# Optimization experiments

Hardware: AMD Instinct MI355X
Metric: run time of the kernel (lower is better)

## Reference

```python
import jax, jax.numpy as jnp
from jax import lax
import numpy as np

N, M, P, K = 2, 16384, 5023, 4
C_PLANE, HP = 32, 256
OUT_DIM = 32


def _harmonic(x):
    # pytorch3d HarmonicEmbedding(n=4, logspace, omega_0=1, append_input=True)
    f = jnp.asarray([1.0, 2.0, 4.0, 8.0], x.dtype)
    e = (x[..., None] * f).reshape(x.shape[:-1] + (-1,))  # [..., 12]
    return jnp.concatenate([jnp.sin(e), jnp.cos(e), x], axis=-1)  # [..., 27]


def _grid_sample2d(img, grid):
    # img [C,H,W], grid [M,2] (x->W, y->H) in [-1,1]; bilinear, zero pad, align_corners=False
    C, H, W = img.shape
    x = (grid[:, 0] + 1.0) * (W / 2.0) - 0.5
    y = (grid[:, 1] + 1.0) * (H / 2.0) - 0.5
    x0 = jnp.floor(x); y0 = jnp.floor(y)
    x1 = x0 + 1.0; y1 = y0 + 1.0
    wx1 = x - x0; wx0 = 1.0 - wx1
    wy1 = y - y0; wy0 = 1.0 - wy1
    def gather(ix, iy):
        valid = ((ix >= 0) & (ix < W) & (iy >= 0) & (iy < H)).astype(img.dtype)
        ixc = jnp.clip(ix, 0, W - 1).astype(jnp.int32)
        iyc = jnp.clip(iy, 0, H - 1).astype(jnp.int32)
        return img[:, iyc, ixc] * valid[None, :]  # [C,M]
    out = (gather(x0, y0) * (wx0 * wy0) + gather(x1, y0) * (wx1 * wy0)
           + gather(x0, y1) * (wx0 * wy1) + gather(x1, y1) * (wx1 * wy1))
    return out.T  # [M,C]


def _forward(coordinates, directions, points_position, tex_tplanes, emb_table,
             pw1, pb1, pw2, pb2, fw1, fb1, fw2, fb2, fw3, fb3, dw, db, rw1, rb1, rw2, rb2):
    c = coordinates
    p = points_position
    # --- triplane sampling (EG3D projections (x,y),(x,z),(z,x)), mean over planes ---
    proj = jnp.stack([c[..., :2],
                      c[..., jnp.array([0, 2])],
                      c[..., jnp.array([2, 0])]], axis=1)  # [N,3,M,2]
    tex = jax.vmap(jax.vmap(_grid_sample2d))(tex_tplanes, proj).mean(axis=1)  # [N,M,32]
    # --- KNN (squared distances, ascending, as pytorch3d knn_points) ---
    d2 = (jnp.sum(c * c, -1)[:, :, None] + jnp.sum(p * p, -1)[:, None, :]
          - 2.0 * jnp.einsum('nmc,npc->nmp', c, p))  # [N,M,P]
    negd, idx = lax.top_k(-d2, K)
    dist = -negd  # [N,M,K]
    nn = jax.vmap(lambda pts, i: pts[i])(p, idx)  # [N,M,K,3]
    pf = emb_table[idx]  # [N,M,K,32]
    rel = c[:, :, None, :] - nn
    rel = rel / jnp.maximum(jnp.linalg.norm(rel, axis=-1, keepdims=True), 1e-12)
    h = jnp.concatenate([pf, _harmonic(rel)], axis=-1)  # [N,M,K,59]
    h = jax.nn.relu(h @ pw1 + pb1) @ pw2 + pb2  # [N,M,K,32]
    w = 1.0 / dist
    w = w / jnp.sum(w, axis=1, keepdims=True)  # dim=1 exactly as in source
    pts_feat = jnp.sum(h * w[..., None], axis=2)  # [N,M,32]
    # --- dense MLP stack ---
    feat = jnp.concatenate([tex, pts_feat], axis=-1)  # [N,M,64]
    feat = jax.nn.relu(feat @ fw1 + fb1)
    feat = jax.nn.relu(feat @ fw2 + fb2)
    feat = feat @ fw3 + fb3  # [N,M,128]
    selector = jnp.all((c > -1.0) & (c < 1.0), axis=-1)  # [N,M]
    raw = (jax.nn.softplus(10.0 * (feat @ dw + db)) / 10.0) * selector[..., None]
    densities = 1.0 - jnp.exp(-raw)
    rays = directions / jnp.maximum(jnp.linalg.norm(directions, axis=-1, keepdims=True), 1e-12)
    rgb = jnp.concatenate([feat, _harmonic(rays)], axis=-1)  # [N,M,155]
    rgb = jax.nn.relu(rgb @ rw1 + rb1) @ rw2 + rb2  # [N,M,OUT_DIM]
    rgb = jnp.concatenate([jax.nn.sigmoid(rgb[..., :3]) * (1.0 + 2 * 0.001) - 0.001,
                           rgb[..., 3:]], axis=-1)
    return densities, rgb, dist


def setup_inputs() -> dict:
    key = jax.random.key(0)
    ks = jax.random.split(key, 16)
    rn = lambda k, s, sc=1.0: jax.random.normal(k, s, jnp.float32) * sc
    def lin(k, i, o):
        k1, k2 = jax.random.split(k)
        return rn(k1, (i, o), 1.0 / np.sqrt(i)), rn(k2, (o,), 0.01)
    coordinates = jax.random.uniform(ks[0], (N, M, 3), jnp.float32)
    directions = rn(ks[1], (N, M, 3))
    points_position = jax.random.uniform(ks[2], (N, P, 3), jnp.float32)
    tex_tplanes = rn(ks[3], (N, 3, C_PLANE, HP, HP))
    emb_table = rn(ks[4], (P, 32), 0.02)
    pw1, pb1 = lin(ks[5], 32 + 27, 64)
    pw2, pb2 = lin(ks[6], 64, 32)
    fw1, fb1 = lin(ks[7], 64, 128)
    fw2, fb2 = lin(ks[8], 128, 128)
    fw3, fb3 = lin(ks[9], 128, 128)
    dw, db = lin(ks[10], 128, 1)
    rw1, rb1 = lin(ks[11], 128 + 27, 64)
    rw2, rb2 = lin(ks[12], 64, OUT_DIM)
    return dict(coordinates=coordinates, directions=directions, points_position=points_position,
                tex_tplanes=tex_tplanes, emb_table=emb_table, pw1=pw1, pb1=pb1, pw2=pw2, pb2=pb2,
                fw1=fw1, fb1=fb1, fw2=fw2, fb2=fb2, fw3=fw3, fb3=fb3, dw=dw, db=db,
                rw1=rw1, rb1=rb1, rw2=rw2, rb2=rb2)


def reference(coordinates, directions, points_position, tex_tplanes, emb_table,
              pw1, pb1, pw2, pb2, fw1, fb1, fw2, fb2, fw3, fb3, dw, db, rw1, rb1, rw2, rb2):
    return _forward(coordinates, directions, points_position, tex_tplanes, emb_table,
                    pw1, pb1, pw2, pb2, fw1, fb1, fw2, fb2, fw3, fb3, dw, db, rw1, rb1, rw2, rb2)
```

## Files before the change

### kernel.cpp

```cpp
#include <hip/hip_runtime.h>
#include <float.h>
#include <math.h>

#define NB 2
#define MQ 16384
#define NQ (NB*MQ)
#define PP 5023
#define KNN 4
#define HPX 256
#define HWSZ (HPX*HPX)

#define OUT_RGB_OFF  ((size_t)NQ)
#define OUT_DIST_OFF ((size_t)NQ + (size_t)NQ*32)

#define WS_SUMS_OFF ((size_t)NQ*KNN*4)
#define WS_PTS4_OFF ((size_t)0x90000)
#define WS_WP_OFF   ((size_t)0xC0000)
#define WS_TEX_OFF  ((size_t)1<<20)

#define WP_PW1 0
#define WP_PW2 1920
#define WP_FW1 2944
#define WP_FW2 7040
#define WP_FW3 15232
#define WP_DW  23424
#define WP_RW1 23488
#define WP_RW2 28480

typedef __attribute__((ext_vector_type(2))) _Float16 half2v;

static __device__ __forceinline__ unsigned int pk2(float a, float b) {
    half2v h; h[0] = (_Float16)a; h[1] = (_Float16)b;
    return __builtin_bit_cast(unsigned int, h);
}
static __device__ __forceinline__ float2 upk(unsigned int u) {
    half2v h = __builtin_bit_cast(half2v, u);
    return make_float2((float)h[0], (float)h[1]);
}
static __device__ __forceinline__ float dot2(unsigned int a, unsigned int b, float c) {
    return __builtin_amdgcn_fdot2(__builtin_bit_cast(half2v, a),
                                  __builtin_bit_cast(half2v, b), c, false);
}

struct PackArgs {
    const float* src[8];
    int off[8]; int din[8]; int dout[8];
};
__global__ __launch_bounds__(256) void k_pack(PackArgs a, unsigned int* wp) {
    const int mid = blockIdx.y;
    const int idx = blockIdx.x * 256 + threadIdx.x;
    const int DIN = a.din[mid], DOUT = a.dout[mid];
    const int din2 = (DIN + 1) >> 1;
    if (idx >= din2 * DOUT) return;
    const int i2 = idx / DOUT, j = idx - i2 * DOUT;
    const float* s = a.src[mid];
    const float lo = s[(2*i2) * DOUT + j];
    const float hi = (2*i2 + 1 < DIN) ? s[(2*i2 + 1) * DOUT + j] : 0.f;
    wp[a.off[mid] + idx] = pk2(lo, hi);
}

__global__ __launch_bounds__(256) void k_pts4(const float* __restrict__ pts,
                                              float4* __restrict__ o) {
    const int i = blockIdx.x * 256 + threadIdx.x;
    if (i >= NB * PP) return;
    const float px = pts[3*i], py = pts[3*i+1], pz = pts[3*i+2];
    o[i] = make_float4(px, py, pz, fmaf(px, px, fmaf(py, py, pz*pz)));
}

__global__ __launch_bounds__(256) void k_transpose(const float* __restrict__ src,
                                                   float* __restrict__ dst) {
    const int tid = threadIdx.x;
    const int b = blockIdx.x;
    const int n3 = b >> 8;
    const int hw = ((b & 255) << 8) + tid;
    const float* s = src + (size_t)n3 * 32 * HWSZ + hw;
    float v[32];
#pragma unroll
    for (int c = 0; c < 32; ++c) v[c] = s[(size_t)c * HWSZ];
    float4* d = (float4*)(dst + ((size_t)n3 * HWSZ + hw) * 32);
#pragma unroll
    for (int c = 0; c < 8; ++c) d[c] = make_float4(v[4*c], v[4*c+1], v[4*c+2], v[4*c+3]);
}

__global__ __launch_bounds__(1024, 2) void k_knn(const float* __restrict__ coords,
                                                 const float4* __restrict__ pts4,
                                                 const float* __restrict__ pts,
                                                 float* __restrict__ odist,
                                                 int* __restrict__ oidx) {
    __shared__ unsigned int KB[16][4][64];
    const int tid  = threadIdx.x;
    const int lane = tid & 63;
    const int w    = __builtin_amdgcn_readfirstlane(tid >> 6);
    const int q0   = blockIdx.x * 64;
    const int q    = q0 + lane;
    const int n    = q0 >> 14;
    const float cx = coords[q*3+0], cy = coords[q*3+1], cz = coords[q*3+2];
    const float cc = fmaf(cx, cx, fmaf(cy, cy, cz*cz));
    const float4* __restrict__ p4 = pts4 + (size_t)n * PP;

    const int chunk  = (PP + 15) / 16;
    const int pstart = w * chunk;
    const int pend   = (pstart + chunk < PP) ? (pstart + chunk) : PP;

    unsigned int k0 = 0xFFFFFFFFu, k1 = 0xFFFFFFFFu, k2 = 0xFFFFFFFFu, k3 = 0xFFFFFFFFu;

#define INS(kb) { \
        unsigned int m2 = ((kb) > k2) ? (kb) : k2;  k3 = (k3 < m2) ? k3 : m2; \
        unsigned int m1 = ((kb) > k1) ? (kb) : k1;  k2 = (k2 < m1) ? k2 : m1; \
        unsigned int m0 = ((kb) > k0) ? (kb) : k0;  k1 = (k1 < m0) ? k1 : m0; \
        k0 = (k0 < (kb)) ? k0 : (kb); }

    int p = pstart;
    for (; p + 8 <= pend; p += 8) {
        float4 P[8];
#pragma unroll
        for (int j = 0; j < 8; ++j) P[j] = p4[p + j];
#pragma unroll
        for (int j = 0; j < 8; ++j) {
            const float dot = fmaf(cx, P[j].x, fmaf(cy, P[j].y, cz * P[j].z));
            float dd = fmaxf(fmaf(-2.0f, dot, cc + P[j].w), 0.f);
            const unsigned int kb = (__float_as_uint(dd) & 0xFFFFE000u) | (unsigned int)(p + j);
            INS(kb)
        }
    }
    for (; p < pend; ++p) {
        const float4 P = p4[p];
        const float dot = fmaf(cx, P.x, fmaf(cy, P.y, cz * P.z));
        float dd = fmaxf(fmaf(-2.0f, dot, cc + P.w), 0.f);
        const unsigned int kb = (__float_as_uint(dd) & 0xFFFFE000u) | (unsigned int)p;
        INS(kb)
    }

    KB[w][0][lane] = k0; KB[w][1][lane] = k1; KB[w][2][lane] = k2; KB[w][3][lane] = k3;
    __syncthreads();

    if (w == 0) {
        unsigned int s0 = 0xFFFFFFFFu, s1 = 0xFFFFFFFFu, s2 = 0xFFFFFFFFu, s3 = 0xFFFFFFFFu;
#pragma unroll
        for (int ww = 0; ww < 16; ++ww)
#pragma unroll
            for (int j = 0; j < 4; ++j) {
                const unsigned int kb = KB[ww][j][lane];
                unsigned int m2 = (kb > s2) ? kb : s2;  s3 = (s3 < m2) ? s3 : m2;
                unsigned int m1 = (kb > s1) ? kb : s1;  s2 = (s2 < m1) ? s2 : m1;
                unsigned int m0 = (kb > s0) ? kb : s0;  s1 = (s1 < m0) ? s1 : m0;
                s0 = (s0 < kb) ? s0 : kb;
            }
        const float* __restrict__ pb = pts + (size_t)n * PP * 3;
        int   id[4] = { (int)(s0 & 0x1FFFu), (int)(s1 & 0x1FFFu),
                        (int)(s2 & 0x1FFFu), (int)(s3 & 0x1FFFu) };
        float dv[4];
#pragma unroll
        for (int j = 0; j < 4; ++j) {
            const float px = pb[3*id[j]+0], py = pb[3*id[j]+1], pz = pb[3*id[j]+2];
            const float dt  = fmaf(cx, px, fmaf(cy, py, cz*pz));
            const float pp2 = fmaf(px, px, fmaf(py, py, pz*pz));
            dv[j] = fmaf(-2.0f, dt, cc + pp2);
        }
#define CSW(a,b) { bool sw = (dv[b] < dv[a]) || (dv[b] == dv[a] && id[b] < id[a]); \
                   if (sw) { float td=dv[a]; dv[a]=dv[b]; dv[b]=td; int ti=id[a]; id[a]=id[b]; id[b]=ti; } }
        CSW(0,1) CSW(2,3) CSW(0,2) CSW(1,3) CSW(1,2)
#undef CSW
        *(float4*)(odist + (size_t)q*4) = make_float4(dv[0], dv[1], dv[2], dv[3]);
        *(int4*)(oidx + (size_t)q*4)    = make_int4(id[0], id[1], id[2], id[3]);
    }
#undef INS
}

__global__ __launch_bounds__(1024) void k_sums(const float* __restrict__ dist,
                                               float* __restrict__ sums) {
    const int b = blockIdx.x;
    const int n = b >> 2, k = b & 3;
    float s = 0.f;
    for (int m = threadIdx.x; m < MQ; m += 1024)
        s += 1.0f / dist[((size_t)n * MQ + m) * 4 + k];
    __shared__ float red[1024];
    red[threadIdx.x] = s;
    __syncthreads();
    for (int off = 512; off > 0; off >>= 1) {
        if (threadIdx.x < off) red[threadIdx.x] += red[threadIdx.x + off];
        __syncthreads();
    }
    if (threadIdx.x == 0) sums[b] = red[0];
}

template<int DIN2, int DOUT, int TILE>
__device__ __forceinline__ void gemv_p(const unsigned int* __restrict__ Xp, int lane,
                                       const unsigned int* __restrict__ Wp,
                                       const float* __restrict__ bias,
                                       int j0, float (&acc)[TILE]) {
#pragma unroll
    for (int u = 0; u < TILE; ++u) acc[u] = bias[j0 + u];
#pragma unroll
    for (int i2 = 0; i2 < DIN2; ++i2) {
        const unsigned int xv = Xp[i2 * 64 + lane];
        const unsigned int* wr = Wp + i2 * DOUT + j0;
#pragma unroll
        for (int u = 0; u < TILE; ++u) acc[u] = dot2(xv, wr[u], acc[u]);
    }
}

static __device__ __forceinline__ float harm_val(int h, float rx, float ry, float rz) {
    if (h >= 27) return 0.f;
    float v;
    if (h < 24) {
        int base = (h < 12) ? h : (h - 12);
        float rv = (base >> 2) == 0 ? rx : ((base >> 2) == 1 ? ry : rz);
        float e = rv * (float)(1 << (base & 3));
        v = (h < 12) ? sinf(e) : cosf(e);
    } else {
        v = (h == 24) ? rx : ((h == 25) ? ry : rz);
    }
    return v;
}

__global__ __launch_bounds__(1024, 2) void k_main(
    const float* __restrict__ coords, const float* __restrict__ dirs,
    const float* __restrict__ pts, const float* __restrict__ tex_raw,
    const float* __restrict__ tex_t, const float* __restrict__ emb,
    const unsigned int* __restrict__ wp,
    const float* __restrict__ pb1, const float* __restrict__ pb2,
    const float* __restrict__ fb1, const float* __restrict__ fb2,
    const float* __restrict__ fb3, const float* __restrict__ db,
    const float* __restrict__ rb1, const float* __restrict__ rb2,
    const int* __restrict__ idxbuf, const float* __restrict__ distbuf,
    const float* __restrict__ sums, float* __restrict__ out, int use_tex_t)
{
    __shared__ unsigned int S[248 * 64];
    const int tid  = threadIdx.x;
    const int lane = tid & 63;
    const int wv   = __builtin_amdgcn_readfirstlane(tid >> 6);
    const int q0   = blockIdx.x * 64;
    const int n    = q0 >> 14;
    const int q    = q0 + lane;

    float tex_acc[2] = {0.f, 0.f};
    {
        const int g = wv;
        const float cx = coords[q*3+0], cy = coords[q*3+1], cz = coords[q*3+2];
#pragma unroll
        for (int pl = 0; pl < 3; ++pl) {
            float gx = (pl == 2) ? cz : cx;
            float gy = (pl == 0) ? cy : ((pl == 1) ? cz : cx);
            float x = (gx + 1.f) * 128.f - 0.5f;
            float y = (gy + 1.f) * 128.f - 0.5f;
            float x0f = floorf(x), y0f = floorf(y);
            float wx1 = x - x0f, wy1 = y - y0f;
            float wx0 = 1.f - wx1, wy0 = 1.f - wy1;
            int x0 = (int)x0f, y0 = (int)y0f;
            int n3 = n * 3 + pl;
            int  xs[4] = { x0, x0+1, x0,   x0+1 };
            int  ys[4] = { y0, y0,   y0+1, y0+1 };
            float wt[4] = { wx0*wy0, wx1*wy0, wx0*wy1, wx1*wy1 };
#pragma unroll
            for (int c = 0; c < 4; ++c) {
                int xi = xs[c], yi = ys[c];
                if (xi >= 0 && xi < HPX && yi >= 0 && yi < HPX) {
                    float wgt = wt[c];
                    if (use_tex_t) {
                        const float2 a = *(const float2*)(tex_t +
                            (((size_t)n3 * HWSZ + (size_t)yi * HPX + xi) * 32 + g * 2));
                        tex_acc[0] = fmaf(wgt, a.x, tex_acc[0]);
                        tex_acc[1] = fmaf(wgt, a.y, tex_acc[1]);
                    } else {
                        size_t base = ((size_t)(n3 * 32 + g * 2)) * HWSZ + (size_t)yi * HPX + xi;
                        tex_acc[0] = fmaf(wgt, tex_raw[base], tex_acc[0]);
                        tex_acc[1] = fmaf(wgt, tex_raw[base + HWSZ], tex_acc[1]);
                    }
                }
            }
        }
        tex_acc[0] *= (1.f / 3.f); tex_acc[1] *= (1.f / 3.f);
    }

    const int kk  = wv & 3;
    const int prt = wv >> 2;

    {
        const int id = idxbuf[(size_t)q*4 + kk];
        const int rb = kk * 30;
        if (prt < 2) {
#pragma unroll
            for (int t = 0; t < 2; ++t) {
                const float4 e = *(const float4*)(emb + (size_t)id * 32 + prt*16 + t*4 + 0)
                    , e2 = *(const float4*)(emb + (size_t)id * 32 + prt*16 + t*4 + 8);
                S[(rb + prt*8 + t*2    )*64 + lane] = pk2(e.x,  e.y);
                S[(rb + prt*8 + t*2 + 1)*64 + lane] = pk2(e.z,  e.w);
                S[(rb + prt*8 + t*2 + 4)*64 + lane] = pk2(e2.x, e2.y);
                S[(rb + prt*8 + t*2 + 5)*64 + lane] = pk2(e2.z, e2.w);
            }
        } else {
            const float cx = coords[q*3+0], cy = coords[q*3+1], cz = coords[q*3+2];
            const float nx = pts[((size_t)n*PP + id)*3 + 0];
            const float ny = pts[((size_t)n*PP + id)*3 + 1];
            const float nz = pts[((size_t)n*PP + id)*3 + 2];
            float rx = cx - nx, ry = cy - ny, rz = cz - nz;
            float nrm = sqrtf(fmaf(rx, rx, fmaf(ry, ry, rz*rz)));
            float inv = 1.f / fmaxf(nrm, 1e-12f);
            rx *= inv; ry *= inv; rz *= inv;
            const int pr0 = (prt == 2) ? 0 : 8;
            const int prn = (prt == 2) ? 8 : 6;
#pragma unroll
            for (int t = 0; t < 8; ++t) {
                if (t < prn) {
                    int pr = pr0 + t;
                    S[(rb + 16 + pr)*64 + lane] =
                        pk2(harm_val(2*pr, rx, ry, rz), harm_val(2*pr + 1, rx, ry, rz));
                }
            }
        }
    }
    __syncthreads();

    {
        float acc[16];
        gemv_p<30, 64, 16>(S + (kk*30)*64, lane, wp + WP_PW1, pb1, prt * 16, acc);
        const int rb = 120 + kk*32 + prt*8;
#pragma unroll
        for (int u = 0; u < 8; ++u)
            S[(rb + u)*64 + lane] = pk2(fmaxf(acc[2*u], 0.f), fmaxf(acc[2*u+1], 0.f));
    }
    __syncthreads();

    {
        float acc[8];
        gemv_p<32, 32, 8>(S + (120 + kk*32)*64, lane, wp + WP_PW2, pb2, prt * 8, acc);
        const float dist = distbuf[(size_t)q*4 + kk];
        const float wk = (1.0f / dist) / sums[n*4 + kk];
        const int rb = kk*16 + prt*4;
#pragma unroll
        for (int u = 0; u < 4; ++u)
            S[(rb + u)*64 + lane] = pk2(wk * acc[2*u], wk * acc[2*u+1]);
    }
    __syncthreads();

    {
        S[(128 + wv)*64 + lane] = pk2(tex_acc[0], tex_acc[1]);
        float a = 0.f, b = 0.f;
#pragma unroll
        for (int k = 0; k < 4; ++k) {
            float2 v = upk(S[(k*16 + wv)*64 + lane]);
            a += v.x; b += v.y;
        }
        S[(144 + wv)*64 + lane] = pk2(a, b);
    }
    __syncthreads();

    {
        float acc[8];
        gemv_p<32, 128, 8>(S + 128*64, lane, wp + WP_FW1, fb1, wv * 8, acc);
#pragma unroll
        for (int u = 0; u < 4; ++u)
            S[(4*wv + u)*64 + lane] = pk2(fmaxf(acc[2*u], 0.f), fmaxf(acc[2*u+1], 0.f));
    }
    __syncthreads();
    {
        float acc[8];
        gemv_p<64, 128, 8>(S, lane, wp + WP_FW2, fb2, wv * 8, acc);
#pragma unroll
        for (int u = 0; u < 4; ++u)
            S[(64 + 4*wv + u)*64 + lane] = pk2(fmaxf(acc[2*u], 0.f), fmaxf(acc[2*u+1], 0.f));
    }
    __syncthreads();
    {
        float acc[8];
        gemv_p<64, 128, 8>(S + 64*64, lane, wp + WP_FW3, fb3, wv * 8, acc);
#pragma unroll
        for (int u = 0; u < 4; ++u)
            S[(4*wv + u)*64 + lane] = pk2(acc[2*u], acc[2*u+1]);
    }
    __syncthreads();
    {
        if (wv < 14) {
            float dx = dirs[q*3+0], dy = dirs[q*3+1], dz = dirs[q*3+2];
            float dn = sqrtf(fmaf(dx, dx, fmaf(dy, dy, dz*dz)));
            float inv = 1.f / fmaxf(dn, 1e-12f);
            dx *= inv; dy *= inv; dz *= inv;
            S[(128 + wv)*64 + lane] = pk2(harm_val(2*wv, dx, dy, dz),
                                          harm_val(2*wv + 1, dx, dy, dz));
        } else if (wv == 15) {
            float z = db[0];
            const unsigned int* dwp = wp + WP_DW;
#pragma unroll
            for (int i2 = 0; i2 < 64; ++i2) z = dot2(S[i2*64 + lane], dwp[i2], z);
            const float cx = coords[q*3+0], cy = coords[q*3+1], cz = coords[q*3+2];
            float selv = (cx > -1.f && cx < 1.f && cy > -1.f && cy < 1.f &&
                          cz > -1.f && cz < 1.f) ? 1.f : 0.f;
            float t10 = 10.f * z;
            float sp = (t10 > 20.f) ? t10 : log1pf(expf(t10));
            float raw = sp * 0.1f * selv;
            out[q] = 1.f - expf(-raw);
        }
    }
    __syncthreads();
    {
        const int j0 = wv * 4;
        float acc[4];
        gemv_p<64, 64, 4>(S, lane, wp + WP_RW1, rb1, j0, acc);
#pragma unroll
        for (int t = 0; t < 14; ++t) {
            const unsigned int xv = S[(128 + t)*64 + lane];
            const unsigned int* wr = wp + WP_RW1 + (64 + t) * 64 + j0;
#pragma unroll
            for (int u = 0; u < 4; ++u) acc[u] = dot2(xv, wr[u], acc[u]);
        }
        S[(64 + 2*wv    )*64 + lane] = pk2(fmaxf(acc[0], 0.f), fmaxf(acc[1], 0.f));
        S[(64 + 2*wv + 1)*64 + lane] = pk2(fmaxf(acc[2], 0.f), fmaxf(acc[3], 0.f));
    }
    __syncthreads();
    {
        float acc[2];
        gemv_p<32, 32, 2>(S + 64*64, lane, wp + WP_RW2, rb2, wv * 2, acc);
#pragma unroll
        for (int u = 0; u < 2; ++u) {
            int j = wv*2 + u;
            float v = acc[u];
            if (j < 3) v = 1.002f * (1.f / (1.f + expf(-v))) - 0.001f;
            out[OUT_RGB_OFF + (size_t)q*32 + j] = v;
        }
    }
}

extern "C" void kernel_launch(void* const* d_in, const int* in_sizes, int n_in,
                              void* d_out, int out_size, void* d_ws, size_t ws_size,
                              hipStream_t stream) {
    (void)in_sizes; (void)n_in; (void)out_size;
    const float* coords = (const float*)d_in[0];
    const float* dirs   = (const float*)d_in[1];
    const float* pts    = (const float*)d_in[2];
    const float* tex    = (const float*)d_in[3];
    const float* emb    = (const float*)d_in[4];
    const float* pw1 = (const float*)d_in[5];  const float* pb1 = (const float*)d_in[6];
    const float* pw2 = (const float*)d_in[7];  const float* pb2 = (const float*)d_in[8];
    const float* fw1 = (const float*)d_in[9];  const float* fb1 = (const float*)d_in[10];
    const float* fw2 = (const float*)d_in[11]; const float* fb2 = (const float*)d_in[12];
    const float* fw3 = (const float*)d_in[13]; const float* fb3 = (const float*)d_in[14];
    const float* dw  = (const float*)d_in[15]; const float* db  = (const float*)d_in[16];
    const float* rw1 = (const float*)d_in[17]; const float* rb1 = (const float*)d_in[18];
    const float* rw2 = (const float*)d_in[19]; const float* rb2 = (const float*)d_in[20];

    float*        out    = (float*)d_out;
    int*          wsidx  = (int*)d_ws;
    float*        wssums = (float*)((char*)d_ws + WS_SUMS_OFF);
    float4*       wspts4 = (float4*)((char*)d_ws + WS_PTS4_OFF);
    unsigned int* wswp   = (unsigned int*)((char*)d_ws + WS_WP_OFF);
    float*        wstex  = (float*)((char*)d_ws + WS_TEX_OFF);

    const size_t need_tex = WS_TEX_OFF + (size_t)6 * HWSZ * 32 * 4;
    const int use_t = (ws_size >= need_tex) ? 1 : 0;

    PackArgs pa;
    pa.src[0] = pw1; pa.off[0] = WP_PW1; pa.din[0] = 59;  pa.dout[0] = 64;
    pa.src[1] = pw2; pa.off[1] = WP_PW2; pa.din[1] = 64;  pa.dout[1] = 32;
    pa.src[2] = fw1; pa.off[2] = WP_FW1; pa.din[2] = 64;  pa.dout[2] = 128;
    pa.src[3] = fw2; pa.off[3] = WP_FW2; pa.din[3] = 128; pa.dout[3] = 128;
    pa.src[4] = fw3; pa.off[4] = WP_FW3; pa.din[4] = 128; pa.dout[4] = 128;
    pa.src[5] = dw;  pa.off[5] = WP_DW;  pa.din[5] = 128; pa.dout[5] = 1;
    pa.src[6] = rw1; pa.off[6] = WP_RW1; pa.din[6] = 155; pa.dout[6] = 64;
    pa.src[7] = rw2; pa.off[7] = WP_RW2; pa.din[7] = 64;  pa.dout[7] = 32;

    k_pack<<<dim3(32, 8), 256, 0, stream>>>(pa, wswp);
    k_pts4<<<(NB*PP + 255)/256, 256, 0, stream>>>(pts, wspts4);
    if (use_t) k_transpose<<<6 * 256, 256, 0, stream>>>(tex, wstex);
    k_knn<<<NQ / 64, 1024, 0, stream>>>(coords, wspts4, pts, out + OUT_DIST_OFF, wsidx);
    k_sums<<<8, 1024, 0, stream>>>(out + OUT_DIST_OFF, wssums);
    k_main<<<NQ / 64, 1024, 0, stream>>>(coords, dirs, pts, tex, wstex, emb,
                                         wswp, pb1, pb2, fb1, fb2, fb3, db, rb1, rb2,
                                         wsidx, out + OUT_DIST_OFF, wssums, out, use_t);
}
```

Measured before the change: 330.4 us.

## Stage KNN points and MLP weights in LDS with double-buffered prefetch

The KNN kernel now loads point chunks cooperatively into shared memory and scans them from LDS rather than each wave streaming from global memory. The main MLP kernel copies weight slices into two shared buffers through register prefetch interleaved with compute, so GEMV weight reads come from LDS instead of scalar or global loads. It also processes the K neighbors two at a time to shrink the activation buffer. This adds many more barriers, a longer serial schedule and more LDS use, which may reduce occupancy.

```diff
diff --git a/kernel.cpp b/kernel.cpp
--- a/kernel.cpp
+++ b/kernel.cpp
@@ -82,11 +82,13 @@
     for (int c = 0; c < 8; ++c) d[c] = make_float4(v[4*c], v[4*c+1], v[4*c+2], v[4*c+3]);
 }
 
+#define KCHUNK 2560
 __global__ __launch_bounds__(1024, 2) void k_knn(const float* __restrict__ coords,
                                                  const float4* __restrict__ pts4,
                                                  const float* __restrict__ pts,
                                                  float* __restrict__ odist,
                                                  int* __restrict__ oidx) {
+    __shared__ float4 SP[KCHUNK];
     __shared__ unsigned int KB[16][4][64];
     const int tid  = threadIdx.x;
     const int lane = tid & 63;
@@ -98,10 +100,6 @@
     const float cc = fmaf(cx, cx, fmaf(cy, cy, cz*cz));
     const float4* __restrict__ p4 = pts4 + (size_t)n * PP;
 
-    const int chunk  = (PP + 15) / 16;
-    const int pstart = w * chunk;
-    const int pend   = (pstart + chunk < PP) ? (pstart + chunk) : PP;
-
     unsigned int k0 = 0xFFFFFFFFu, k1 = 0xFFFFFFFFu, k2 = 0xFFFFFFFFu, k3 = 0xFFFFFFFFu;
 
 #define INS(kb) { \
@@ -110,26 +108,27 @@
         unsigned int m0 = ((kb) > k0) ? (kb) : k0;  k1 = (k1 < m0) ? k1 : m0; \
         k0 = (k0 < (kb)) ? k0 : (kb); }
 
-    int p = pstart;
-    for (; p + 8 <= pend; p += 8) {
-        float4 P[8];
-#pragma unroll
-        for (int j = 0; j < 8; ++j) P[j] = p4[p + j];
-#pragma unroll
-        for (int j = 0; j < 8; ++j) {
-            const float dot = fmaf(cx, P[j].x, fmaf(cy, P[j].y, cz * P[j].z));
-            float dd = fmaxf(fmaf(-2.0f, dot, cc + P[j].w), 0.f);
-            const unsigned int kb = (__float_as_uint(dd) & 0xFFFFE000u) | (unsigned int)(p + j);
+#pragma unroll 1
+    for (int half = 0; half < 2; ++half) {
+        const int base = half * KCHUNK;
+        const int cnt  = (PP - base < KCHUNK) ? (PP - base) : KCHUNK;
+        __syncthreads();
+        for (int i = tid; i < cnt; i += 1024) SP[i] = p4[base + i];
+        __syncthreads();
+        const int per = (cnt + 15) >> 4;
+        const int s0 = w * per;
+        const int s1 = (s0 + per < cnt) ? (s0 + per) : cnt;
+#pragma unroll 4
+        for (int j = s0; j < s1; ++j) {
+            const float4 P = SP[j];
+            const float dot = fmaf(cx, P.x, fmaf(cy, P.y, cz * P.z));
+            float dd = fmaxf(fmaf(-2.0f, dot, cc + P.w), 0.f);
+            const unsigned int kb = (__float_as_uint(dd) & 0xFFFFE000u)
+                                    | (unsigned int)(base + j);
             INS(kb)
         }
     }
-    for (; p < pend; ++p) {
-        const float4 P = p4[p];
-        const float dot = fmaf(cx, P.x, fmaf(cy, P.y, cz * P.z));
-        float dd = fmaxf(fmaf(-2.0f, dot, cc + P.w), 0.f);
-        const unsigned int kb = (__float_as_uint(dd) & 0xFFFFE000u) | (unsigned int)p;
-        INS(kb)
-    }
+#undef INS
 
     KB[w][0][lane] = k0; KB[w][1][lane] = k1; KB[w][2][lane] = k2; KB[w][3][lane] = k3;
     __syncthreads();
@@ -164,7 +163,6 @@
         *(float4*)(odist + (size_t)q*4) = make_float4(dv[0], dv[1], dv[2], dv[3]);
         *(int4*)(oidx + (size_t)q*4)    = make_int4(id[0], id[1], id[2], id[3]);
     }
-#undef INS
 }
 
 __global__ __launch_bounds__(1024) void k_sums(const float* __restrict__ dist,
@@ -185,8 +183,8 @@
 }
 
 template<int DIN2, int DOUT, int TILE>
-__device__ __forceinline__ void gemv_p(const unsigned int* __restrict__ Xp, int lane,
-                                       const unsigned int* __restrict__ Wp,
+__device__ __forceinline__ void gemv_p(const unsigned int* Xp, int lane,
+                                       const unsigned int* Wl,
                                        const float* __restrict__ bias,
                                        int j0, float (&acc)[TILE]) {
 #pragma unroll
@@ -194,7 +192,19 @@
 #pragma unroll
     for (int i2 = 0; i2 < DIN2; ++i2) {
         const unsigned int xv = Xp[i2 * 64 + lane];
-        const unsigned int* wr = Wp + i2 * DOUT + j0;
+        const unsigned int* wr = Wl + i2 * DOUT + j0;
+#pragma unroll
+        for (int u = 0; u < TILE; ++u) acc[u] = dot2(xv, wr[u], acc[u]);
+    }
+}
+template<int DIN2, int DOUT, int TILE>
+__device__ __forceinline__ void gemv_acc(const unsigned int* Xp, int lane,
+                                         const unsigned int* Wl,
+                                         int j0, float (&acc)[TILE]) {
+#pragma unroll
+    for (int i2 = 0; i2 < DIN2; ++i2) {
+        const unsigned int xv = Xp[i2 * 64 + lane];
+        const unsigned int* wr = Wl + i2 * DOUT + j0;
 #pragma unroll
         for (int u = 0; u < TILE; ++u) acc[u] = dot2(xv, wr[u], acc[u]);
     }
@@ -226,13 +236,17 @@
     const int* __restrict__ idxbuf, const float* __restrict__ distbuf,
     const float* __restrict__ sums, float* __restrict__ out, int use_tex_t)
 {
-    __shared__ unsigned int S[248 * 64];
+    __shared__ unsigned int S[188 * 64];
+    __shared__ unsigned int WBa[2048];
+    __shared__ unsigned int WBb[2048];
     const int tid  = threadIdx.x;
     const int lane = tid & 63;
     const int wv   = __builtin_amdgcn_readfirstlane(tid >> 6);
     const int q0   = blockIdx.x * 64;
     const int n    = q0 >> 14;
     const int q    = q0 + lane;
+
+    unsigned int pa0, pa1, pb0_, pb1_;
 
     float tex_acc[2] = {0.f, 0.f};
     {
@@ -273,116 +287,210 @@
         tex_acc[0] *= (1.f / 3.f); tex_acc[1] *= (1.f / 3.f);
     }
 
-    const int kk  = wv & 3;
-    const int prt = wv >> 2;
-
+#define PF_LOAD(r0, r1, off, len) { \
+        r0 = (tid < (len)) ? wp[(off) + tid] : 0u; \
+        r1 = (tid + 1024 < (len)) ? wp[(off) + tid + 1024] : 0u; }
+#define PF_STORE(buf, r0, r1, len) { \
+        if (tid < (len)) buf[tid] = r0; \
+        if (tid + 1024 < (len)) buf[tid + 1024] = r1; }
+
+    const int kk2 = wv & 1;
+    const int sl  = wv >> 1;
+
+#define PHASE_A(pp) { \
+        const int k = (pp)*2 + kk2; \
+        const int id = idxbuf[(size_t)q*4 + k]; \
+        const int xb = 64 + kk2*30; \
+        if (sl < 4) { \
+            const float4 e0 = *(const float4*)(emb + (size_t)id * 32 + sl*8); \
+            const float4 e1 = *(const float4*)(emb + (size_t)id * 32 + sl*8 + 4); \
+            S[(xb + sl*4 + 0)*64 + lane] = pk2(e0.x, e0.y); \
+            S[(xb + sl*4 + 1)*64 + lane] = pk2(e0.z, e0.w); \
+            S[(xb + sl*4 + 2)*64 + lane] = pk2(e1.x, e1.y); \
+            S[(xb + sl*4 + 3)*64 + lane] = pk2(e1.z, e1.w); \
+        } else { \
+            const float cx = coords[q*3+0], cy = coords[q*3+1], cz = coords[q*3+2]; \
+            const float nx = pts[((size_t)n*PP + id)*3 + 0]; \
+            const float ny = pts[((size_t)n*PP + id)*3 + 1]; \
+            const float nz = pts[((size_t)n*PP + id)*3 + 2]; \
+            float rx = cx - nx, ry = cy - ny, rz = cz - nz; \
+            float nrm = sqrtf(fmaf(rx, rx, fmaf(ry, ry, rz*rz))); \
+            float inv = 1.f / fmaxf(nrm, 1e-12f); \
+            rx *= inv; ry *= inv; rz *= inv; \
+            const int pr0 = (sl == 4) ? 0 : (sl == 5) ? 4 : (sl == 6) ? 8 : 11; \
+            const int prn = (sl <= 5) ? 4 : 3; \
+            for (int t = 0; t < 4; ++t) if (t < prn) { \
+                int pr = pr0 + t; \
+                S[(xb + 16 + pr)*64 + lane] = \
+                    pk2(harm_val(2*pr, rx, ry, rz), harm_val(2*pr + 1, rx, ry, rz)); \
+            } \
+        } }
+
+#define PHASE_B() { \
+        float acc[8]; \
+        gemv_p<30, 64, 8>(S + (64 + kk2*30)*64, lane, WBa, pb1, sl*8, acc); \
+        const int rb = 124 + kk2*32 + sl*4; \
+        for (int u = 0; u < 4; ++u) \
+            S[(rb + u)*64 + lane] = pk2(fmaxf(acc[2*u], 0.f), fmaxf(acc[2*u+1], 0.f)); }
+
+#define PHASE_C(pp) { \
+        float acc[4]; \
+        gemv_p<32, 32, 4>(S + (124 + kk2*32)*64, lane, WBb, pb2, sl*4, acc); \
+        const int k = (pp)*2 + kk2; \
+        const float dist = distbuf[(size_t)q*4 + k]; \
+        const float wk = (1.0f / dist) / sums[n*4 + k]; \
+        const int rb = k*16 + sl*2; \
+        S[(rb + 0)*64 + lane] = pk2(wk * acc[0], wk * acc[1]); \
+        S[(rb + 1)*64 + lane] = pk2(wk * acc[2], wk * acc[3]); }
+
+    PF_LOAD(pa0, pa1, WP_PW1, 1920)
+    PHASE_A(0)
+    PF_STORE(WBa, pa0, pa1, 1920)
+    PF_LOAD(pb0_, pb1_, WP_PW2, 1024)
+    __syncthreads();
+    PHASE_B()
+    PF_STORE(WBb, pb0_, pb1_, 1024)
+    PF_LOAD(pa0, pa1, WP_FW1, 2048)
+    __syncthreads();
+    PHASE_C(0)
+    PHASE_A(1)
+    __syncthreads();
+    PHASE_B()
+    PF_LOAD(pb0_, pb1_, WP_FW1 + 2048, 2048)
+    __syncthreads();
+    PHASE_C(1)
+    PF_STORE(WBa, pa0, pa1, 2048)
+    __syncthreads();
     {
-        const int id = idxbuf[(size_t)q*4 + kk];
-        const int rb = kk * 30;
-        if (prt < 2) {
-#pragma unroll
-            for (int t = 0; t < 2; ++t) {
-                const float4 e = *(const float4*)(emb + (size_t)id * 32 + prt*16 + t*4 + 0)
-                    , e2 = *(const float4*)(emb + (size_t)id * 32 + prt*16 + t*4 + 8);
-                S[(rb + prt*8 + t*2    )*64 + lane] = pk2(e.x,  e.y);
-                S[(rb + prt*8 + t*2 + 1)*64 + lane] = pk2(e.z,  e.w);
-                S[(rb + prt*8 + t*2 + 4)*64 + lane] = pk2(e2.x, e2.y);
-                S[(rb + prt*8 + t*2 + 5)*64 + lane] = pk2(e2.z, e2.w);
-            }
-        } else {
-            const float cx = coords[q*3+0], cy = coords[q*3+1], cz = coords[q*3+2];
-            const float nx = pts[((size_t)n*PP + id)*3 + 0];
-            const float ny = pts[((size_t)n*PP + id)*3 + 1];
-            const float nz = pts[((size_t)n*PP + id)*3 + 2];
-            float rx = cx - nx, ry = cy - ny, rz = cz - nz;
-            float nrm = sqrtf(fmaf(rx, rx, fmaf(ry, ry, rz*rz)));
-            float inv = 1.f / fmaxf(nrm, 1e-12f);
-            rx *= inv; ry *= inv; rz *= inv;
-            const int pr0 = (prt == 2) ? 0 : 8;
-            const int prn = (prt == 2) ? 8 : 6;
-#pragma unroll
-            for (int t = 0; t < 8; ++t) {
-                if (t < prn) {
-                    int pr = pr0 + t;
-                    S[(rb + 16 + pr)*64 + lane] =
-                        pk2(harm_val(2*pr, rx, ry, rz), harm_val(2*pr + 1, rx, ry, rz));
-                }
-            }
-        }
-    }
-    __syncthreads();
-
-    {
-        float acc[16];
-        gemv_p<30, 64, 16>(S + (kk*30)*64, lane, wp + WP_PW1, pb1, prt * 16, acc);
-        const int rb = 120 + kk*32 + prt*8;
-#pragma unroll
-        for (int u = 0; u < 8; ++u)
-            S[(rb + u)*64 + lane] = pk2(fmaxf(acc[2*u], 0.f), fmaxf(acc[2*u+1], 0.f));
-    }
-    __syncthreads();
-
-    {
-        float acc[8];
-        gemv_p<32, 32, 8>(S + (120 + kk*32)*64, lane, wp + WP_PW2, pb2, prt * 8, acc);
-        const float dist = distbuf[(size_t)q*4 + kk];
-        const float wk = (1.0f / dist) / sums[n*4 + kk];
-        const int rb = kk*16 + prt*4;
-#pragma unroll
-        for (int u = 0; u < 4; ++u)
-            S[(rb + u)*64 + lane] = pk2(wk * acc[2*u], wk * acc[2*u+1]);
-    }
-    __syncthreads();
-
-    {
-        S[(128 + wv)*64 + lane] = pk2(tex_acc[0], tex_acc[1]);
+        S[(64 + wv)*64 + lane] = pk2(tex_acc[0], tex_acc[1]);
         float a = 0.f, b = 0.f;
 #pragma unroll
         for (int k = 0; k < 4; ++k) {
             float2 v = upk(S[(k*16 + wv)*64 + lane]);
             a += v.x; b += v.y;
         }
-        S[(144 + wv)*64 + lane] = pk2(a, b);
-    }
-    __syncthreads();
-
+        S[(80 + wv)*64 + lane] = pk2(a, b);
+    }
+    PF_STORE(WBb, pb0_, pb1_, 2048)
+    PF_LOAD(pa0, pa1, WP_FW2, 2048)
+    __syncthreads();
+    float accE[8];
+#pragma unroll
+    for (int u = 0; u < 8; ++u) accE[u] = fb1[wv*8 + u];
+    gemv_acc<16, 128, 8>(S + 64*64, lane, WBa, wv*8, accE);
+    PF_LOAD(pb0_, pb1_, WP_FW2 + 2048, 2048)
+    __syncthreads();
+    gemv_acc<16, 128, 8>(S + 80*64, lane, WBb, wv*8, accE);
+#pragma unroll
+    for (int u = 0; u < 4; ++u)
+        S[(96 + wv*4 + u)*64 + lane] = pk2(fmaxf(accE[2*u], 0.f), fmaxf(accE[2*u+1], 0.f));
+    PF_STORE(WBa, pa0, pa1, 2048)
+    __syncthreads();
+    float accF[8];
+#pragma unroll
+    for (int u = 0; u < 8; ++u) accF[u] = fb2[wv*8 + u];
+    gemv_acc<16, 128, 8>(S + 96*64, lane, WBa, wv*8, accF);
+    PF_STORE(WBb, pb0_, pb1_, 2048)
+    PF_LOAD(pa0, pa1, WP_FW2 + 4096, 2048)
+    __syncthreads();
+    gemv_acc<16, 128, 8>(S + 112*64, lane, WBb, wv*8, accF);
+    PF_STORE(WBa, pa0, pa1, 2048)
+    PF_LOAD(pb0_, pb1_, WP_FW2 + 6144, 2048)
+    __syncthreads();
+    gemv_acc<16, 128, 8>(S + 128*64, lane, WBa, wv*8, accF);
+    PF_STORE(WBb, pb0_, pb1_, 2048)
+    PF_LOAD(pa0, pa1, WP_FW3, 2048)
+    __syncthreads();
+    gemv_acc<16, 128, 8>(S + 144*64, lane, WBb, wv*8, accF);
+#pragma unroll
+    for (int u = 0; u < 4; ++u)
+        S[(wv*4 + u)*64 + lane] = pk2(fmaxf(accF[2*u], 0.f), fmaxf(accF[2*u+1], 0.f));
+    PF_STORE(WBa, pa0, pa1, 2048)
+    PF_LOAD(pb0_, pb1_, WP_FW3 + 2048, 2048)
+    __syncthreads();
+    float accG[8];
+#pragma unroll
+    for (int u = 0; u < 8; ++u) accG[u] = fb3[wv*8 + u];
+    gemv_acc<16, 128, 8>(S + 0*64, lane, WBa, wv*8, accG);
+    PF_STORE(WBb, pb0_, pb1_, 2048)
+    PF_LOAD(pa0, pa1, WP_FW3 + 4096, 2048)
+    __syncthreads();
+    gemv_acc<16, 128, 8>(S + 16*64, lane, WBb, wv*8, accG);
+    PF_STORE(WBa, pa0, pa1, 2048)
+    PF_LOAD(pb0_, pb1_, WP_FW3 + 6144, 2048)
+    __syncthreads();
+    gemv_acc<16, 128, 8>(S + 32*64, lane, WBa, wv*8, accG);
+    PF_STORE(WBb, pb0_, pb1_, 2048)
+    PF_LOAD(pa0, pa1, WP_RW1, 1664)
+    __syncthreads();
+    gemv_acc<16, 128, 8>(S + 48*64, lane, WBb, wv*8, accG);
+#pragma unroll
+    for (int u = 0; u < 4; ++u)
+        S[(96 + wv*4 + u)*64 + lane] = pk2(accG[2*u], accG[2*u+1]);
+    if (wv < 14) {
+        float dx = dirs[q*3+0], dy = dirs[q*3+1], dz = dirs[q*3+2];
+        float dn = sqrtf(fmaf(dx, dx, fmaf(dy, dy, dz*dz)));
+        float inv = 1.f / fmaxf(dn, 1e-12f);
+        dx *= inv; dy *= inv; dz *= inv;
+        S[(64 + wv)*64 + lane] = pk2(harm_val(2*wv, dx, dy, dz),
+                                     harm_val(2*wv + 1, dx, dy, dz));
+    }
+    PF_STORE(WBa, pa0, pa1, 1664)
+    PF_LOAD(pb0_, pb1_, WP_RW1 + 1664, 1664)
+    __syncthreads();
+    const int j0r = wv * 4;
+    float accI[4];
+#pragma unroll
+    for (int u = 0; u < 4; ++u) accI[u] = rb1[j0r + u];
+#pragma unroll 1
+    for (int i2 = 0; i2 < 26; ++i2) {
+        const unsigned int xv = S[(96 + i2)*64 + lane];
+        const unsigned int* wr = WBa + i2*64 + j0r;
+#pragma unroll
+        for (int u = 0; u < 4; ++u) accI[u] = dot2(xv, wr[u], accI[u]);
+    }
+    PF_STORE(WBb, pb0_, pb1_, 1664)
+    PF_LOAD(pa0, pa1, WP_RW1 + 3328, 1664)
+    __syncthreads();
+#pragma unroll 1
+    for (int i2 = 26; i2 < 52; ++i2) {
+        const unsigned int xv = S[(96 + i2)*64 + lane];
+        const unsigned int* wr = WBb + (i2 - 26)*64 + j0r;
+#pragma unroll
+        for (int u = 0; u < 4; ++u) accI[u] = dot2(xv, wr[u], accI[u]);
+    }
+    PF_STORE(WBa, pa0, pa1, 1664)
+    PF_LOAD(pb0_, pb1_, WP_RW2, 1024)
+    unsigned int pd0 = (tid < 64) ? wp[WP_DW + tid] : 0u;
+    __syncthreads();
+#pragma unroll 1
+    for (int i2 = 52; i2 < 78; ++i2) {
+        const int xr = (i2 < 64) ? (96 + i2) : (64 + (i2 - 64));
+        const unsigned int xv = S[xr*64 + lane];
+        const unsigned int* wr = WBa + (i2 - 52)*64 + j0r;
+#pragma unroll
+        for (int u = 0; u < 4; ++u) accI[u] = dot2(xv, wr[u], accI[u]);
+    }
+    S[(wv*2 + 0)*64 + lane] = pk2(fmaxf(accI[0], 0.f), fmaxf(accI[1], 0.f));
+    S[(wv*2 + 1)*64 + lane] = pk2(fmaxf(accI[2], 0.f), fmaxf(accI[3], 0.f));
+    PF_STORE(WBb, pb0_, pb1_, 1024)
+    if (tid < 64) WBb[1024 + tid] = pd0;
+    __syncthreads();
     {
-        float acc[8];
-        gemv_p<32, 128, 8>(S + 128*64, lane, wp + WP_FW1, fb1, wv * 8, acc);
-#pragma unroll
-        for (int u = 0; u < 4; ++u)
-            S[(4*wv + u)*64 + lane] = pk2(fmaxf(acc[2*u], 0.f), fmaxf(acc[2*u+1], 0.f));
-    }
-    __syncthreads();
-    {
-        float acc[8];
-        gemv_p<64, 128, 8>(S, lane, wp + WP_FW2, fb2, wv * 8, acc);
-#pragma unroll
-        for (int u = 0; u < 4; ++u)
-            S[(64 + 4*wv + u)*64 + lane] = pk2(fmaxf(acc[2*u], 0.f), fmaxf(acc[2*u+1], 0.f));
-    }
-    __syncthreads();
-    {
-        float acc[8];
-        gemv_p<64, 128, 8>(S + 64*64, lane, wp + WP_FW3, fb3, wv * 8, acc);
-#pragma unroll
-        for (int u = 0; u < 4; ++u)
-            S[(4*wv + u)*64 + lane] = pk2(acc[2*u], acc[2*u+1]);
-    }
-    __syncthreads();
-    {
-        if (wv < 14) {
-            float dx = dirs[q*3+0], dy = dirs[q*3+1], dz = dirs[q*3+2];
-            float dn = sqrtf(fmaf(dx, dx, fmaf(dy, dy, dz*dz)));
-            float inv = 1.f / fmaxf(dn, 1e-12f);
-            dx *= inv; dy *= inv; dz *= inv;
-            S[(128 + wv)*64 + lane] = pk2(harm_val(2*wv, dx, dy, dz),
-                                          harm_val(2*wv + 1, dx, dy, dz));
-        } else if (wv == 15) {
+        float acc[2];
+        gemv_p<32, 32, 2>(S, lane, WBb, rb2, wv*2, acc);
+#pragma unroll
+        for (int u = 0; u < 2; ++u) {
+            int j = wv*2 + u;
+            float v = acc[u];
+            if (j < 3) v = 1.002f * (1.f / (1.f + expf(-v))) - 0.001f;
+            out[OUT_RGB_OFF + (size_t)q*32 + j] = v;
+        }
+        if (wv == 15) {
             float z = db[0];
-            const unsigned int* dwp = wp + WP_DW;
-#pragma unroll
-            for (int i2 = 0; i2 < 64; ++i2) z = dot2(S[i2*64 + lane], dwp[i2], z);
+#pragma unroll 1
+            for (int i2 = 0; i2 < 64; ++i2)
+                z = dot2(S[(96 + i2)*64 + lane], WBb[1024 + i2], z);
             const float cx = coords[q*3+0], cy = coords[q*3+1], cz = coords[q*3+2];
             float selv = (cx > -1.f && cx < 1.f && cy > -1.f && cy < 1.f &&
                           cz > -1.f && cz < 1.f) ? 1.f : 0.f;
@@ -392,33 +500,11 @@
             out[q] = 1.f - expf(-raw);
         }
     }
-    __syncthreads();
-    {
-        const int j0 = wv * 4;
-        float acc[4];
-        gemv_p<64, 64, 4>(S, lane, wp + WP_RW1, rb1, j0, acc);
-#pragma unroll
-        for (int t = 0; t < 14; ++t) {
-            const unsigned int xv = S[(128 + t)*64 + lane];
-            const unsigned int* wr = wp + WP_RW1 + (64 + t) * 64 + j0;
-#pragma unroll
-            for (int u = 0; u < 4; ++u) acc[u] = dot2(xv, wr[u], acc[u]);
-        }
-        S[(64 + 2*wv    )*64 + lane] = pk2(fmaxf(acc[0], 0.f), fmaxf(acc[1], 0.f));
-        S[(64 + 2*wv + 1)*64 + lane] = pk2(fmaxf(acc[2], 0.f), fmaxf(acc[3], 0.f));
-    }
-    __syncthreads();
-    {
-        float acc[2];
-        gemv_p<32, 32, 2>(S + 64*64, lane, wp + WP_RW2, rb2, wv * 2, acc);
-#pragma unroll
-        for (int u = 0; u < 2; ++u) {
-            int j = wv*2 + u;
-            float v = acc[u];
-            if (j < 3) v = 1.002f * (1.f / (1.f + expf(-v))) - 0.001f;
-            out[OUT_RGB_OFF + (size_t)q*32 + j] = v;
-        }
-    }
+#undef PF_LOAD
+#undef PF_STORE
+#undef PHASE_A
+#undef PHASE_B
+#undef PHASE_C
 }
 
 extern "C" void kernel_launch(void* const* d_in, const int* in_sizes, int n_in,
```

New measurement: 329.1 us. About the same (-0.4%).
